# Kernel tuning notes

Hardware: AMD Instinct MI355X
Metric: run time of the kernel (lower is better)

The kernel has to match this reference:

```python
import math
import jax, jax.numpy as jnp
import numpy as np

LN_EPS = 1e-5


def _layernorm(x, g, b):
    m = jnp.mean(x, axis=-1, keepdims=True)
    v = jnp.var(x, axis=-1, keepdims=True)
    return (x - m) / jnp.sqrt(v + LN_EPS) * g + b


def setup_inputs() -> dict:
    key = jax.random.key(0)
    ks = jax.random.split(key, 14)
    B, C, H, W = 8, 96, 224, 224
    dim, hidden = 96, int(96 * 4.0)

    def lin(k, i, o):
        return jax.random.normal(k, (i, o), jnp.float32) * 0.02

    return {
        "x": jax.random.normal(ks[0], (B, C, H, W), jnp.float32),
        "entropy_map": jax.random.uniform(ks[1], (B, 1, H, W), jnp.float32),
        "beta": jnp.float32(1.0),
        "wq": lin(ks[2], dim, dim), "bq": jnp.zeros((dim,), jnp.float32),
        "wk": lin(ks[3], dim, dim), "bk": jnp.zeros((dim,), jnp.float32),
        "wv": lin(ks[4], dim, dim), "bv": jnp.zeros((dim,), jnp.float32),
        "wo": lin(ks[5], dim, dim), "bo": jnp.zeros((dim,), jnp.float32),
        "ln1_g": jnp.ones((dim,), jnp.float32), "ln1_b": jnp.zeros((dim,), jnp.float32),
        "ln2_g": jnp.ones((dim,), jnp.float32), "ln2_b": jnp.zeros((dim,), jnp.float32),
        "w_fc1": lin(ks[6], dim, hidden), "b_fc1": jnp.zeros((hidden,), jnp.float32),
        "w_fc2": lin(ks[7], hidden, dim), "b_fc2": jnp.zeros((dim,), jnp.float32),
    }


def reference(x, entropy_map, beta, wq, bq, wk, bk, wv, bv, wo, bo,
              ln1_g, ln1_b, ln2_g, ln2_b, w_fc1, b_fc1, w_fc2, b_fc2):
    B, C, H, W = x.shape
    ws = 7
    num_heads = 4
    hd = C // num_heads
    nHw, nWw = H // ws, W // ws
    N = ws * ws

    # (B,C,H,W) -> (B,H,W,C), norm1
    xt = jnp.transpose(x, (0, 2, 3, 1))
    xn = _layernorm(xt, ln1_g, ln1_b)

    # window partition -> (B*nW, N, C)
    xw = xn.reshape(B, nHw, ws, nWw, ws, C).transpose(0, 1, 3, 2, 4, 5).reshape(-1, N, C)
    ew = entropy_map.transpose(0, 2, 3, 1).reshape(B, nHw, ws, nWw, ws, 1)
    ew = ew.transpose(0, 1, 3, 2, 4, 5).reshape(-1, N, 1)  # (Bw, N, 1)

    Bw = xw.shape[0]
    q = (jnp.einsum('bnc,cd->bnd', xw, wq) + bq).reshape(Bw, N, num_heads, hd).transpose(0, 2, 1, 3)
    k = (jnp.einsum('bnc,cd->bnd', xw, wk) + bk).reshape(Bw, N, num_heads, hd).transpose(0, 2, 1, 3)
    v = (jnp.einsum('bnc,cd->bnd', xw, wv) + bv).reshape(Bw, N, num_heads, hd).transpose(0, 2, 1, 3)

    scores = jnp.einsum('bhqd,bhkd->bhqk', q, k) / math.sqrt(hd)
    attn = jax.nn.softmax(scores, axis=-1)

    # entropy gating: per-query factor (Bw,1,N,1), then renormalize over keys
    gating = jnp.exp(-beta * ew)[:, None, :, :]
    attn = attn * gating
    attn = attn / (jnp.sum(attn, axis=-1, keepdims=True) + 1e-9)

    out = jnp.einsum('bhqk,bhkd->bhqd', attn, v).transpose(0, 2, 1, 3).reshape(Bw, N, C)
    out = jnp.einsum('bnc,cd->bnd', out, wo) + bo

    # window merge -> (B,H,W,C)
    out = out.reshape(B, nHw, nWw, ws, ws, C).transpose(0, 1, 3, 2, 4, 5).reshape(B, H, W, C)

    x_res = xt + out  # (B,H,W,C)

    # MLP branch
    xn2 = _layernorm(x_res, ln2_g, ln2_b)
    h = jax.nn.gelu(jnp.einsum('bhwc,cd->bhwd', xn2, w_fc1) + b_fc1, approximate=False)
    mlp_out = jnp.einsum('bhwd,dc->bhwc', h, w_fc2) + b_fc2

    x_out = x_res + mlp_out
    return jnp.transpose(x_out, (0, 3, 1, 2))  # (B,C,H,W)
```

## Files before the change

kernel.cpp:

```cpp
#include <hip/hip_runtime.h>
#include <math.h>

typedef __attribute__((ext_vector_type(8))) short short8;
typedef __attribute__((ext_vector_type(4))) float f32x4;
typedef __attribute__((ext_vector_type(4))) unsigned int uint4v;

struct __align__(8) U2 { unsigned int x, y; };

#define DEVI static __device__ __forceinline__

DEVI unsigned pk1(float f){ unsigned u = __float_as_uint(f); return (u + 0x7fffu + ((u>>16)&1u)) >> 16; }
DEVI unsigned pk2(float a, float b){ return pk1(a) | (pk1(b) << 16); }
DEVI float bfu(unsigned hs){ return __uint_as_float((hs & 0xffffu) << 16); }

DEVI short8 lds8(const unsigned short* p){
  union { short8 v; U2 u[2]; } f;
  f.u[0] = *(const U2*)p;
  f.u[1] = *(const U2*)(p + 4);
  return f.v;
}
DEVI short8 mk8(unsigned a, unsigned b, unsigned c, unsigned d){
  union { short8 v; unsigned u[4]; } f; f.u[0]=a; f.u[1]=b; f.u[2]=c; f.u[3]=d; return f.v;
}
DEVI short8 zero8(){ return mk8(0,0,0,0); }
DEVI short8 gfrag(const unsigned short* p){ union { short8 v; uint4v u; } f; f.u = *(const uint4v*)p; return f.v; }
DEVI f32x4 MFMA(short8 a, short8 b, f32x4 c){ return __builtin_amdgcn_mfma_f32_16x16x32_bf16(a, b, c, 0, 0, 0); }
DEVI void st2(unsigned short* p, unsigned lo, unsigned hi){ U2 t; t.x=lo; t.y=hi; *(U2*)p = t; }

__global__ __launch_bounds__(256) void prep_kernel(
    const float* __restrict__ wq, const float* __restrict__ wk,
    const float* __restrict__ wv, const float* __restrict__ wo,
    const float* __restrict__ w1, const float* __restrict__ w2,
    unsigned short* __restrict__ wfr)
{
  int i = blockIdx.x * 256 + threadIdx.x;
  if (i >= 110592) return;
  int j = i & 7, lane = (i >> 3) & 63, fr = i >> 9;
  int ln = lane & 15, lg = lane >> 4;
  float v;
  if (fr < 18)      { int s = fr;       int mt = s/3,  kb = s%3;  v = wq[(32*kb + 8*lg + j)*96  + 16*mt + ln]; }
  else if (fr < 36) { int s = fr - 18;  int mt = s/3,  kb = s%3;  v = wk[(32*kb + 8*lg + j)*96  + 16*mt + ln]; }
  else if (fr < 54) { int s = fr - 36;  int nt = s/3,  kb = s%3;  v = wv[(32*kb + 8*lg + j)*96  + 16*nt + ln]; }
  else if (fr < 72) { int s = fr - 54;  int mt = s/3,  kb = s%3;  v = wo[(32*kb + 8*lg + j)*96  + 16*mt + ln]; }
  else if (fr < 144){ int s = fr - 72;  int mt = s/3,  kb = s%3;  v = w1[(32*kb + 8*lg + j)*384 + 16*mt + ln]; }
  else              { int s = fr - 144; int mt = s/12, kb = s%12; v = w2[(32*kb + 8*lg + j)*96  + 16*mt + ln]; }
  wfr[i] = (unsigned short)pk1(v);
}

__global__ __launch_bounds__(256, 3) void attn_kernel(
    const float* __restrict__ x, const float* __restrict__ emap,
    const float* __restrict__ beta_p,
    const float* __restrict__ bq, const float* __restrict__ bk,
    const float* __restrict__ bv, const float* __restrict__ bo,
    const float* __restrict__ g1, const float* __restrict__ b1,
    const unsigned short* __restrict__ wfr,
    unsigned short* __restrict__ xres)
{
  __shared__ __align__(16) char smem[52800];
  unsigned short* XN = (unsigned short*)(smem);
  unsigned short* QS = (unsigned short*)(smem + 12800);
  unsigned short* KS = (unsigned short*)(smem + 25600);
  unsigned short* VT = (unsigned short*)(smem + 38400);
  float* EWF = (float*)(smem + 52544);

  const int tid = threadIdx.x;
  const int lane = tid & 63;
  const int w = tid >> 6, lg = lane >> 4, ln = lane & 15;

  int bid = blockIdx.x;
  int bw  = ((bid & 7) << 10) | (bid >> 3);
  const int b  = bw >> 10;
  const int rr = bw & 1023;
  const int h0 = (rr >> 5) * 7;
  const int w0 = (rr & 31) * 7;

  for (int i = tid; i < 8*68; i += 256) VT[(96 + i/68)*68 + i%68] = 0;
  if (tid < 64)
    EWF[tid] = (tid < 49) ? emap[(size_t)b*50176 + (size_t)(h0 + tid/7)*224 + w0 + tid%7] : 0.f;

  {
    const int t = 16*w + ln;
    float xv[24];
    if (t < 49){
      size_t pixloc = (size_t)(h0 + t/7)*224 + w0 + t%7;
      const float* xp = x + (size_t)(b*96 + 24*lg)*50176 + pixloc;
#pragma unroll
      for (int i = 0; i < 24; ++i) xv[i] = xp[(size_t)i*50176];
    } else {
#pragma unroll
      for (int i = 0; i < 24; ++i) xv[i] = 0.f;
    }
    float s = 0.f, s2 = 0.f;
#pragma unroll
    for (int i = 0; i < 24; ++i){ s += xv[i]; s2 += xv[i]*xv[i]; }
    s  += __shfl_xor(s, 16);  s  += __shfl_xor(s, 32);
    s2 += __shfl_xor(s2, 16); s2 += __shfl_xor(s2, 32);
    float m = s * (1.f/96.f);
    float var = s2 * (1.f/96.f) - m*m;
    float rstd = rsqrtf(var + 1e-5f);
    unsigned* w32 = (unsigned*)(XN + t*100 + 24*lg);
    if (t < 49){
#pragma unroll
      for (int i = 0; i < 12; ++i){
        int c = 24*lg + 2*i;
        w32[i] = pk2((xv[2*i]   - m)*rstd*g1[c]   + b1[c],
                     (xv[2*i+1] - m)*rstd*g1[c+1] + b1[c+1]);
      }
    } else {
#pragma unroll
      for (int i = 0; i < 12; ++i) w32[i] = 0;
    }
  }
  __syncthreads();

  {
    short8 bx0 = lds8(XN + (16*w+ln)*100 + 0  + 8*lg);
    short8 bx1 = lds8(XN + (16*w+ln)*100 + 32 + 8*lg);
    short8 bx2 = lds8(XN + (16*w+ln)*100 + 64 + 8*lg);
#pragma unroll
    for (int mt = 0; mt < 6; ++mt){
      int d0 = 16*mt + 4*lg;
      f32x4 aq, ak;
#pragma unroll
      for (int r = 0; r < 4; ++r){ aq[r] = bq[d0+r]; ak[r] = bk[d0+r]; }
      aq = MFMA(gfrag(wfr +        (mt*3+0)*512 + lane*8), bx0, aq);
      aq = MFMA(gfrag(wfr +        (mt*3+1)*512 + lane*8), bx1, aq);
      aq = MFMA(gfrag(wfr +        (mt*3+2)*512 + lane*8), bx2, aq);
      ak = MFMA(gfrag(wfr + 9216 + (mt*3+0)*512 + lane*8), bx0, ak);
      ak = MFMA(gfrag(wfr + 9216 + (mt*3+1)*512 + lane*8), bx1, ak);
      ak = MFMA(gfrag(wfr + 9216 + (mt*3+2)*512 + lane*8), bx2, ak);
      st2(QS + (16*w+ln)*100 + d0, pk2(aq[0],aq[1]), pk2(aq[2],aq[3]));
      st2(KS + (16*w+ln)*100 + d0, pk2(ak[0],ak[1]), pk2(ak[2],ak[3]));
    }
#pragma unroll
    for (int f = 0; f < 6; ++f){
      int fl = f*4 + w;
      int mt = fl / 6, nt = fl % 6;
      float bvv = bv[16*nt + ln];
      f32x4 av; av[0]=bvv; av[1]=bvv; av[2]=bvv; av[3]=bvv;
#pragma unroll
      for (int kb = 0; kb < 3; ++kb)
        av = MFMA(lds8(XN + (16*mt+ln)*100 + 32*kb + 8*lg),
                  gfrag(wfr + 18432 + (nt*3+kb)*512 + lane*8), av);
      st2(VT + (16*nt+ln)*68 + 16*mt + 4*lg, pk2(av[0],av[1]), pk2(av[2],av[3]));
    }
  }
  __syncthreads();

  const float beta  = beta_p[0];
  const float scale = 0.20412414523193150818f;
  const float gq    = __expf(-beta * EWF[16*w + ln]);
  const int  srcA   = ((lg & 1) << 5) + ln;
  const int  srcB   = srcA + 16;
  const bool hi     = (lg >= 2);

#pragma unroll
  for (int h = 0; h < 4; ++h){
    short8 bqf = (lg < 3) ? lds8(QS + (16*w+ln)*100 + 24*h + 8*lg) : zero8();
    f32x4 sva[4];
#pragma unroll
    for (int mt = 0; mt < 4; ++mt){
      f32x4 z; z[0]=0.f; z[1]=0.f; z[2]=0.f; z[3]=0.f;
      short8 af = (lg < 3) ? lds8(KS + (16*mt+ln)*100 + 24*h + 8*lg) : zero8();
      sva[mt] = MFMA(af, bqf, z);
    }
    float vv[16]; float mx = -3e38f;
#pragma unroll
    for (int mt = 0; mt < 4; ++mt)
#pragma unroll
      for (int r = 0; r < 4; ++r){
        int key = 16*mt + 4*lg + r;
        float v = (key <= 48) ? sva[mt][r]*scale : -3e38f;
        vv[mt*4+r] = v; mx = fmaxf(mx, v);
      }
    mx = fmaxf(mx, __shfl_xor(mx, 16));
    mx = fmaxf(mx, __shfl_xor(mx, 32));
    float ssum = 0.f;
#pragma unroll
    for (int i = 0; i < 16; ++i){ float e = __expf(vv[i] - mx); vv[i] = e; ssum += e; }
    ssum += __shfl_xor(ssum, 16);
    ssum += __shfl_xor(ssum, 32);
    float inv = gq / (ssum * (gq + 1e-9f));

    unsigned pu[4][2];
#pragma unroll
    for (int mt = 0; mt < 4; ++mt){
      pu[mt][0] = pk2(vv[4*mt+0]*inv, vv[4*mt+1]*inv);
      pu[mt][1] = pk2(vv[4*mt+2]*inv, vv[4*mt+3]*inv);
    }
    unsigned a00=__shfl(pu[0][0],srcA), a01=__shfl(pu[0][1],srcA);
    unsigned a10=__shfl(pu[1][0],srcA), a11=__shfl(pu[1][1],srcA);
    unsigned b00=__shfl(pu[0][0],srcB), b01=__shfl(pu[0][1],srcB);
    unsigned b10=__shfl(pu[1][0],srcB), b11=__shfl(pu[1][1],srcB);
    short8 pf0 = mk8(hi?a10:a00, hi?a11:a01, hi?b10:b00, hi?b11:b01);
    unsigned c00=__shfl(pu[2][0],srcA), c01=__shfl(pu[2][1],srcA);
    unsigned c10=__shfl(pu[3][0],srcA), c11=__shfl(pu[3][1],srcA);
    unsigned d00=__shfl(pu[2][0],srcB), d01=__shfl(pu[2][1],srcB);
    unsigned d10=__shfl(pu[3][0],srcB), d11=__shfl(pu[3][1],srcB);
    short8 pf1 = mk8(hi?c10:c00, hi?c11:c01, hi?d10:d00, hi?d11:d01);

#pragma unroll
    for (int mt = 0; mt < 2; ++mt){
      f32x4 pv; pv[0]=0.f; pv[1]=0.f; pv[2]=0.f; pv[3]=0.f;
      pv = MFMA(lds8(VT + (24*h+16*mt+ln)*68 + 0  + 8*lg), pf0, pv);
      pv = MFMA(lds8(VT + (24*h+16*mt+ln)*68 + 32 + 8*lg), pf1, pv);
      if (!(mt == 1 && lg >= 2))
        st2(XN + (16*w+ln)*100 + 24*h + 16*mt + 4*lg, pk2(pv[0],pv[1]), pk2(pv[2],pv[3]));
    }
  }

  {
    f32x4 po[6];
#pragma unroll
    for (int mt = 0; mt < 6; ++mt){
      int c0 = 16*mt + 4*lg;
#pragma unroll
      for (int r = 0; r < 4; ++r) po[mt][r] = bo[c0+r];
    }
#pragma unroll
    for (int kb = 0; kb < 3; ++kb){
      short8 bf_ = lds8(XN + (16*w+ln)*100 + 32*kb + 8*lg);
#pragma unroll
      for (int mt = 0; mt < 6; ++mt)
        po[mt] = MFMA(gfrag(wfr + 27648 + (mt*3+kb)*512 + lane*8), bf_, po[mt]);
    }
    const int t = 16*w + ln;
    if (t < 49){
      size_t pixloc = (size_t)(h0 + t/7)*224 + w0 + t%7;
      const float* xp = x + (size_t)b*96*50176 + pixloc;
      unsigned short* xo = xres + ((size_t)b*50176 + pixloc)*96;
#pragma unroll
      for (int mt = 0; mt < 6; ++mt){
        int c0 = 16*mt + 4*lg;
        float r0 = po[mt][0] + xp[(size_t)(c0+0)*50176];
        float r1 = po[mt][1] + xp[(size_t)(c0+1)*50176];
        float r2 = po[mt][2] + xp[(size_t)(c0+2)*50176];
        float r3 = po[mt][3] + xp[(size_t)(c0+3)*50176];
        st2(xo + c0, pk2(r0,r1), pk2(r2,r3));
      }
    }
  }
}

__global__ __launch_bounds__(256, 4) void mlp_kernel(
    const unsigned short* __restrict__ xres,
    const float* __restrict__ g2, const float* __restrict__ b2,
    const float* __restrict__ bf1, const float* __restrict__ bf2,
    const unsigned short* __restrict__ wfr,
    float* __restrict__ out)
{
  __shared__ __align__(16) unsigned short XH[4][4800];
  const int tid = threadIdx.x, lane = tid & 63, w = tid >> 6;
  const int lg = lane >> 4, ln = lane & 15;
  unsigned short* XN2 = &XH[w][0];
  unsigned short* HS  = &XH[w][1600];

  const int tile = blockIdx.x*4 + w;
  const size_t p0 = (size_t)tile * 16;
  const int bimg = (int)(p0 / 50176);
  const size_t pixin = p0 - (size_t)bimg*50176;

  {
    const unsigned* xp = (const unsigned*)(xres + (p0 + (size_t)ln)*96 + 24*lg);
    float xv[24];
#pragma unroll
    for (int i = 0; i < 12; ++i){
      unsigned u = xp[i];
      xv[2*i] = bfu(u); xv[2*i+1] = bfu(u >> 16);
    }
    float s = 0.f, s2 = 0.f;
#pragma unroll
    for (int i = 0; i < 24; ++i){ s += xv[i]; s2 += xv[i]*xv[i]; }
    s  += __shfl_xor(s, 16);  s  += __shfl_xor(s, 32);
    s2 += __shfl_xor(s2, 16); s2 += __shfl_xor(s2, 32);
    float m = s * (1.f/96.f);
    float var = s2 * (1.f/96.f) - m*m;
    float rstd = rsqrtf(var + 1e-5f);
    unsigned* w32 = (unsigned*)(XN2 + ln*100 + 24*lg);
#pragma unroll
    for (int i = 0; i < 12; ++i){
      int c = 24*lg + 2*i;
      w32[i] = pk2((xv[2*i]   - m)*rstd*g2[c]   + b2[c],
                   (xv[2*i+1] - m)*rstd*g2[c+1] + b2[c+1]);
    }
  }

  f32x4 oacc[6];
#pragma unroll
  for (int mt = 0; mt < 6; ++mt){
    int c0 = 16*mt + 4*lg;
#pragma unroll
    for (int r = 0; r < 4; ++r) oacc[mt][r] = bf2[c0+r];
  }

  short8 bxx0 = lds8(XN2 + ln*100 + 0  + 8*lg);
  short8 bxx1 = lds8(XN2 + ln*100 + 32 + 8*lg);
  short8 bxx2 = lds8(XN2 + ln*100 + 64 + 8*lg);

#pragma unroll
  for (int p = 0; p < 2; ++p){
#pragma unroll
    for (int mt = 0; mt < 12; ++mt){
      int hg = p*192 + 16*mt + 4*lg;
      f32x4 ha;
#pragma unroll
      for (int r = 0; r < 4; ++r) ha[r] = bf1[hg+r];
      ha = MFMA(gfrag(wfr + 36864 + ((p*12+mt)*3+0)*512 + lane*8), bxx0, ha);
      ha = MFMA(gfrag(wfr + 36864 + ((p*12+mt)*3+1)*512 + lane*8), bxx1, ha);
      ha = MFMA(gfrag(wfr + 36864 + ((p*12+mt)*3+2)*512 + lane*8), bxx2, ha);
      float e0 = 0.5f*ha[0]*(1.f + erff(ha[0]*0.70710678118654752f));
      float e1 = 0.5f*ha[1]*(1.f + erff(ha[1]*0.70710678118654752f));
      float e2 = 0.5f*ha[2]*(1.f + erff(ha[2]*0.70710678118654752f));
      float e3 = 0.5f*ha[3]*(1.f + erff(ha[3]*0.70710678118654752f));
      st2(HS + ln*200 + 16*mt + 4*lg, pk2(e0,e1), pk2(e2,e3));
    }
#pragma unroll
    for (int kb = 0; kb < 6; ++kb){
      short8 bh = lds8(HS + ln*200 + 32*kb + 8*lg);
#pragma unroll
      for (int mt = 0; mt < 6; ++mt)
        oacc[mt] = MFMA(gfrag(wfr + 73728 + (mt*12 + p*6 + kb)*512 + lane*8), bh, oacc[mt]);
    }
  }

  {
    const unsigned short* xr = xres + (p0 + (size_t)ln)*96;
    float* ob = out + (size_t)bimg*96*50176 + pixin + ln;
#pragma unroll
    for (int mt = 0; mt < 6; ++mt){
      int c0 = 16*mt + 4*lg;
      U2 rv = *(const U2*)(xr + c0);
      ob[(size_t)(c0+0)*50176] = oacc[mt][0] + bfu(rv.x);
      ob[(size_t)(c0+1)*50176] = oacc[mt][1] + bfu(rv.x >> 16);
      ob[(size_t)(c0+2)*50176] = oacc[mt][2] + bfu(rv.y);
      ob[(size_t)(c0+3)*50176] = oacc[mt][3] + bfu(rv.y >> 16);
    }
  }
}

extern "C" void kernel_launch(void* const* d_in, const int* in_sizes, int n_in,
                              void* d_out, int out_size, void* d_ws, size_t ws_size,
                              hipStream_t stream) {
  const float* x    = (const float*)d_in[0];
  const float* emap = (const float*)d_in[1];
  const float* beta = (const float*)d_in[2];
  const float* wq   = (const float*)d_in[3];
  const float* bq   = (const float*)d_in[4];
  const float* wk   = (const float*)d_in[5];
  const float* bk   = (const float*)d_in[6];
  const float* wv   = (const float*)d_in[7];
  const float* bv   = (const float*)d_in[8];
  const float* wo   = (const float*)d_in[9];
  const float* bo   = (const float*)d_in[10];
  const float* g1   = (const float*)d_in[11];
  const float* b1   = (const float*)d_in[12];
  const float* g2   = (const float*)d_in[13];
  const float* b2   = (const float*)d_in[14];
  const float* w1   = (const float*)d_in[15];
  const float* bf1  = (const float*)d_in[16];
  const float* w2   = (const float*)d_in[17];
  const float* bf2  = (const float*)d_in[18];

  float* out = (float*)d_out;
  unsigned short* wfr  = (unsigned short*)d_ws;
  unsigned short* xres = (unsigned short*)((char*)d_ws + 262144);

  prep_kernel<<<dim3(432), dim3(256), 0, stream>>>(wq, wk, wv, wo, w1, w2, wfr);
  attn_kernel<<<dim3(8192), dim3(256), 0, stream>>>(
      x, emap, beta, bq, bk, bv, bo, g1, b1, wfr, xres);
  mlp_kernel<<<dim3(6272), dim3(256), 0, stream>>>(
      xres, g2, b2, bf1, bf2, wfr, out);
}
```

Before: 421.6 us.

## Keep Q in registers, shrink LDS for occupancy, use tanh-form GELU

Q projections now stay in registers and are rearranged into MFMA B-fragments with lane shuffles, so the Q shared-memory buffer goes away. The entropy gate value is loaded straight into a register, which removes the EWF buffer. Together these cut LDS from about 52.8KB to 39.7KB and raise the occupancy hint from 3 to 4 blocks per CU. The MLP replaces erf-based GELU with the tanh approximation written as a sigmoid using a fast reciprocal. That approximation differs slightly from the exact GELU the reference uses, though the error is small next to the bf16 rounding already present.

```diff
diff --git a/kernel.cpp b/kernel.cpp
--- a/kernel.cpp
+++ b/kernel.cpp
@@ -26,6 +26,12 @@
 DEVI short8 gfrag(const unsigned short* p){ union { short8 v; uint4v u; } f; f.u = *(const uint4v*)p; return f.v; }
 DEVI f32x4 MFMA(short8 a, short8 b, f32x4 c){ return __builtin_amdgcn_mfma_f32_16x16x32_bf16(a, b, c, 0, 0, 0); }
 DEVI void st2(unsigned short* p, unsigned lo, unsigned hi){ U2 t; t.x=lo; t.y=hi; *(U2*)p = t; }
+
+DEVI float fastrcp(float x){ float r; asm("v_rcp_f32 %0, %1" : "=v"(r) : "v"(x)); return r; }
+DEVI float gelu_f(float v){
+  float z2 = fmaf(v*v*v, -0.07135481627f, -1.5957691216f*v);
+  return v * fastrcp(1.f + __expf(z2));
+}
 
 __global__ __launch_bounds__(256) void prep_kernel(
     const float* __restrict__ wq, const float* __restrict__ wk,
@@ -47,7 +53,7 @@
   wfr[i] = (unsigned short)pk1(v);
 }
 
-__global__ __launch_bounds__(256, 3) void attn_kernel(
+__global__ __launch_bounds__(256, 4) void attn_kernel(
     const float* __restrict__ x, const float* __restrict__ emap,
     const float* __restrict__ beta_p,
     const float* __restrict__ bq, const float* __restrict__ bk,
@@ -56,12 +62,10 @@
     const unsigned short* __restrict__ wfr,
     unsigned short* __restrict__ xres)
 {
-  __shared__ __align__(16) char smem[52800];
+  __shared__ __align__(16) char smem[39744];
   unsigned short* XN = (unsigned short*)(smem);
-  unsigned short* QS = (unsigned short*)(smem + 12800);
-  unsigned short* KS = (unsigned short*)(smem + 25600);
-  unsigned short* VT = (unsigned short*)(smem + 38400);
-  float* EWF = (float*)(smem + 52544);
+  unsigned short* KS = (unsigned short*)(smem + 12800);
+  unsigned short* VT = (unsigned short*)(smem + 25600);
 
   const int tid = threadIdx.x;
   const int lane = tid & 63;
@@ -75,9 +79,8 @@
   const int w0 = (rr & 31) * 7;
 
   for (int i = tid; i < 8*68; i += 256) VT[(96 + i/68)*68 + i%68] = 0;
-  if (tid < 64)
-    EWF[tid] = (tid < 49) ? emap[(size_t)b*50176 + (size_t)(h0 + tid/7)*224 + w0 + tid%7] : 0.f;
-
+
+  float ewv = 0.f;
   {
     const int t = 16*w + ln;
     float xv[24];
@@ -86,6 +89,7 @@
       const float* xp = x + (size_t)(b*96 + 24*lg)*50176 + pixloc;
 #pragma unroll
       for (int i = 0; i < 24; ++i) xv[i] = xp[(size_t)i*50176];
+      ewv = emap[(size_t)b*50176 + pixloc];
     } else {
 #pragma unroll
       for (int i = 0; i < 24; ++i) xv[i] = 0.f;
@@ -113,6 +117,7 @@
   }
   __syncthreads();
 
+  unsigned qp[6][2];
   {
     short8 bx0 = lds8(XN + (16*w+ln)*100 + 0  + 8*lg);
     short8 bx1 = lds8(XN + (16*w+ln)*100 + 32 + 8*lg);
@@ -129,7 +134,8 @@
       ak = MFMA(gfrag(wfr + 9216 + (mt*3+0)*512 + lane*8), bx0, ak);
       ak = MFMA(gfrag(wfr + 9216 + (mt*3+1)*512 + lane*8), bx1, ak);
       ak = MFMA(gfrag(wfr + 9216 + (mt*3+2)*512 + lane*8), bx2, ak);
-      st2(QS + (16*w+ln)*100 + d0, pk2(aq[0],aq[1]), pk2(aq[2],aq[3]));
+      qp[mt][0] = pk2(aq[0],aq[1]);
+      qp[mt][1] = pk2(aq[2],aq[3]);
       st2(KS + (16*w+ln)*100 + d0, pk2(ak[0],ak[1]), pk2(ak[2],ak[3]));
     }
 #pragma unroll
@@ -149,14 +155,25 @@
 
   const float beta  = beta_p[0];
   const float scale = 0.20412414523193150818f;
-  const float gq    = __expf(-beta * EWF[16*w + ln]);
-  const int  srcA   = ((lg & 1) << 5) + ln;
-  const int  srcB   = srcA + 16;
-  const bool hi     = (lg >= 2);
+  const float gq    = __expf(-beta * ewv);
+  const int  psrcA  = ((lg & 1) << 5) + ln;
+  const int  psrcB  = psrcA + 16;
+  const bool phi    = (lg >= 2);
 
 #pragma unroll
   for (int h = 0; h < 4; ++h){
-    short8 bqf = (lg < 3) ? lds8(QS + (16*w+ln)*100 + 24*h + 8*lg) : zero8();
+    const int mlo = (6*h) >> 2, mhi = mlo + 1;
+    const int thr = (h & 1) ? 1 : 2;
+    int par  = (3*h + lg) & 1;
+    int srcA = (par << 5) + ln;
+    int srcB = srcA + 16;
+    unsigned lA0 = __shfl(qp[mlo][0], srcA), lA1 = __shfl(qp[mlo][1], srcA);
+    unsigned hA0 = __shfl(qp[mhi][0], srcA), hA1 = __shfl(qp[mhi][1], srcA);
+    unsigned lB0 = __shfl(qp[mlo][0], srcB), lB1 = __shfl(qp[mlo][1], srcB);
+    unsigned hB0 = __shfl(qp[mhi][0], srcB), hB1 = __shfl(qp[mhi][1], srcB);
+    bool uh = (lg >= thr);
+    short8 bqf = (lg < 3) ? mk8(uh?hA0:lA0, uh?hA1:lA1, uh?hB0:lB0, uh?hB1:lB1) : zero8();
+
     f32x4 sva[4];
 #pragma unroll
     for (int mt = 0; mt < 4; ++mt){
@@ -188,16 +205,16 @@
       pu[mt][0] = pk2(vv[4*mt+0]*inv, vv[4*mt+1]*inv);
       pu[mt][1] = pk2(vv[4*mt+2]*inv, vv[4*mt+3]*inv);
     }
-    unsigned a00=__shfl(pu[0][0],srcA), a01=__shfl(pu[0][1],srcA);
-    unsigned a10=__shfl(pu[1][0],srcA), a11=__shfl(pu[1][1],srcA);
-    unsigned b00=__shfl(pu[0][0],srcB), b01=__shfl(pu[0][1],srcB);
-    unsigned b10=__shfl(pu[1][0],srcB), b11=__shfl(pu[1][1],srcB);
-    short8 pf0 = mk8(hi?a10:a00, hi?a11:a01, hi?b10:b00, hi?b11:b01);
-    unsigned c00=__shfl(pu[2][0],srcA), c01=__shfl(pu[2][1],srcA);
-    unsigned c10=__shfl(pu[3][0],srcA), c11=__shfl(pu[3][1],srcA);
-    unsigned d00=__shfl(pu[2][0],srcB), d01=__shfl(pu[2][1],srcB);
-    unsigned d10=__shfl(pu[3][0],srcB), d11=__shfl(pu[3][1],srcB);
-    short8 pf1 = mk8(hi?c10:c00, hi?c11:c01, hi?d10:d00, hi?d11:d01);
+    unsigned a00=__shfl(pu[0][0],psrcA), a01=__shfl(pu[0][1],psrcA);
+    unsigned a10=__shfl(pu[1][0],psrcA), a11=__shfl(pu[1][1],psrcA);
+    unsigned b00=__shfl(pu[0][0],psrcB), b01=__shfl(pu[0][1],psrcB);
+    unsigned b10=__shfl(pu[1][0],psrcB), b11=__shfl(pu[1][1],psrcB);
+    short8 pf0 = mk8(phi?a10:a00, phi?a11:a01, phi?b10:b00, phi?b11:b01);
+    unsigned c00=__shfl(pu[2][0],psrcA), c01=__shfl(pu[2][1],psrcA);
+    unsigned c10=__shfl(pu[3][0],psrcA), c11=__shfl(pu[3][1],psrcA);
+    unsigned d00=__shfl(pu[2][0],psrcB), d01=__shfl(pu[2][1],psrcB);
+    unsigned d10=__shfl(pu[3][0],psrcB), d11=__shfl(pu[3][1],psrcB);
+    short8 pf1 = mk8(phi?c10:c00, phi?c11:c01, phi?d10:d00, phi?d11:d01);
 
 #pragma unroll
     for (int mt = 0; mt < 2; ++mt){
@@ -308,11 +325,8 @@
       ha = MFMA(gfrag(wfr + 36864 + ((p*12+mt)*3+0)*512 + lane*8), bxx0, ha);
       ha = MFMA(gfrag(wfr + 36864 + ((p*12+mt)*3+1)*512 + lane*8), bxx1, ha);
       ha = MFMA(gfrag(wfr + 36864 + ((p*12+mt)*3+2)*512 + lane*8), bxx2, ha);
-      float e0 = 0.5f*ha[0]*(1.f + erff(ha[0]*0.70710678118654752f));
-      float e1 = 0.5f*ha[1]*(1.f + erff(ha[1]*0.70710678118654752f));
-      float e2 = 0.5f*ha[2]*(1.f + erff(ha[2]*0.70710678118654752f));
-      float e3 = 0.5f*ha[3]*(1.f + erff(ha[3]*0.70710678118654752f));
-      st2(HS + ln*200 + 16*mt + 4*lg, pk2(e0,e1), pk2(e2,e3));
+      st2(HS + ln*200 + 16*mt + 4*lg,
+          pk2(gelu_f(ha[0]), gelu_f(ha[1])), pk2(gelu_f(ha[2]), gelu_f(ha[3])));
     }
 #pragma unroll
     for (int kb = 0; kb < 6; ++kb){
```

Result: no change. 429.9 us (+2.0%).
